# Performance work log

Measured on AMD Instinct MI355X. Metric: run time of the kernel, lower is better.

The kernel has to match this reference:

```python
import jax, jax.numpy as jnp
import numpy as np

N_NODES = 20000
N_EDGES = 320000
IN_DIM = 256
OUT_DIM = 256
N_HEADS = 4
D_K = OUT_DIM // N_HEADS
N_NTYPES = 4
N_RELS = 8
SQRT_DK = float(np.sqrt(D_K))


def setup_inputs() -> dict:
    key = jax.random.key(0)
    ks = jax.random.split(key, 12)
    xav = lambda k, shape, fan: jax.random.normal(k, shape, jnp.float32) * (1.0 / np.sqrt(fan))
    return {
        "h": jax.random.normal(ks[0], (N_NODES, IN_DIM), jnp.float32),
        "k_linears": xav(ks[1], (N_NTYPES, IN_DIM, OUT_DIM), IN_DIM),
        "q_linears": xav(ks[2], (N_NTYPES, IN_DIM, OUT_DIM), IN_DIM),
        "v_linears": xav(ks[3], (N_NTYPES, IN_DIM, OUT_DIM), IN_DIM),
        "a_linears": xav(ks[4], (N_NTYPES, OUT_DIM, OUT_DIM), OUT_DIM),
        "relation_att": xav(ks[5], (N_RELS, N_HEADS, D_K, D_K), D_K),
        "relation_msg": xav(ks[6], (N_RELS, N_HEADS, D_K, D_K), D_K),
        "relation_pri": jnp.ones((N_RELS, N_HEADS), jnp.float32),
        "skip": jnp.ones((N_NTYPES,), jnp.float32),
        "node_type": jax.random.randint(ks[7], (N_NODES,), 0, N_NTYPES),
        "etype": jnp.sort(jax.random.randint(ks[8], (N_EDGES,), 0, N_RELS)),
        "row_idx": jax.random.randint(ks[9], (N_EDGES,), 0, N_NODES),
        "col_idx": jax.random.randint(ks[10], (N_EDGES,), 0, N_NODES),
    }


def _typed_matmul(x, W, node_type):
    # x: [N, in], W: [T, in, out] -> per-node-type projection [N, out]
    all_t = jnp.einsum("ni,tio->tno", x, W)  # [T, N, out]
    return all_t[node_type, jnp.arange(x.shape[0])]


def reference(h, k_linears, q_linears, v_linears, a_linears,
              relation_att, relation_msg, relation_pri, skip,
              node_type, etype, row_idx, col_idx):
    n = h.shape[0]
    # per-node-type K/Q/V projections -> [N, H, d_k]
    k = _typed_matmul(h, k_linears, node_type).reshape(n, N_HEADS, D_K)
    q = _typed_matmul(h, q_linears, node_type).reshape(n, N_HEADS, D_K)
    v = _typed_matmul(h, v_linears, node_type).reshape(n, N_HEADS, D_K)

    # per-relation transforms computed at node granularity, gathered per edge
    q_att = jnp.einsum("nhd,rhde->rnhe", q, relation_att)  # [R, N, H, d_k]
    v_msg = jnp.einsum("nhd,rhde->rnhe", v, relation_msg)  # [R, N, H, d_k]

    aw_q_edge = q_att[etype, col_idx]   # [E, H, d_k]  (dst-side q transformed by rel att)
    msg_edge = v_msg[etype, row_idx]    # [E, H, d_k]  (src-side v transformed by rel msg)

    # attention score: <rel_att @ q_dst, k_src> * pri_r / sqrt(d_k)  -> [E, H]
    attn_score = jnp.sum(aw_q_edge * k[row_idx], axis=-1)
    score = attn_score * (relation_pri[etype] / SQRT_DK)

    # edge softmax over incoming edges of each destination node
    m = jax.ops.segment_max(score, col_idx, num_segments=n)       # [N, H]
    ex = jnp.exp(score - m[col_idx])                              # [E, H]
    denom = jax.ops.segment_sum(ex, col_idx, num_segments=n)      # [N, H]
    alpha = ex / denom[col_idx]                                   # [E, H]

    agg = jax.ops.segment_sum(alpha[..., None] * msg_edge, col_idx,
                              num_segments=n)                     # [N, H, d_k]
    agg = agg.reshape(n, OUT_DIM)

    # output per-node-type projection scaled by sigmoid(skip[type])
    out = _typed_matmul(agg, a_linears, node_type)
    out = jax.nn.sigmoid(skip)[node_type][:, None] * out
    return out
```

## Files before the change

### kernel.cpp

```cpp
#include <hip/hip_runtime.h>

static constexpr int NN  = 20000;
static constexpr int NE  = 320000;
static constexpr int NTY = 4;
static constexpr int NRL = 8;
static constexpr int NB  = NRL * NN;

static constexpr int ZB = (NB + NN * 4 + 255) / 256;
static constexpr int HB = NN * 64 / 256;
static constexpr int WB = 4 * 768;
static constexpr int AB = 4 * 256;
static constexpr int RB = 32 * 4096 / 256;
static constexpr int CB = (NN + 255) / 256;

typedef short bf16x8 __attribute__((ext_vector_type(8)));
typedef float f32x4  __attribute__((ext_vector_type(4)));
typedef unsigned short u16x4 __attribute__((ext_vector_type(4)));

__device__ __forceinline__ unsigned short f2bf(float f) {
  unsigned u = __float_as_uint(f);
  u += 0x7fffu + ((u >> 16) & 1u);
  return (unsigned short)(u >> 16);
}
__device__ __forceinline__ float bf2f(unsigned short b) {
  return __uint_as_float(((unsigned)b) << 16);
}
__device__ __forceinline__ f32x4 mfma16(bf16x8 a, bf16x8 b, f32x4 c) {
  return __builtin_amdgcn_mfma_f32_16x16x32_bf16(a, b, c, 0, 0, 0);
}

__global__ void k_tcount(const int* __restrict__ ntype, int* __restrict__ c4p) {
  __shared__ int c[4];
  if (threadIdx.x < 4) c[threadIdx.x] = 0;
  __syncthreads();
  int i = blockIdx.x * 256 + threadIdx.x;
  if (i < NN) atomicAdd(&c[ntype[i]], 1);
  __syncthreads();
  if (threadIdx.x < 4) c4p[blockIdx.x * 4 + threadIdx.x] = c[threadIdx.x];
}
__global__ void k_meta(const int* __restrict__ c4p, int* toff, int* ncur,
                       int* mt_t, int* mt_m, int* gcnt) {
  __shared__ int c4[4];
  __shared__ int ts[5];
  if (threadIdx.x < 4) {
    int s = 0;
    for (int b = 0; b < CB; ++b) s += c4p[b * 4 + threadIdx.x];
    c4[threadIdx.x] = s;
  }
  __syncthreads();
  if (threadIdx.x == 0) {
    int s = 0, s2 = 0;
    for (int t = 0; t < NTY; ++t) {
      toff[t] = s; ncur[t] = s; s += c4[t];
      ts[t] = s2; s2 += (c4[t] + 15) >> 4;
    }
    toff[NTY] = s; ts[NTY] = s2; gcnt[0] = s2;
  }
  __syncthreads();
  int nmt = ts[4];
  for (int i = threadIdx.x; i < nmt; i += 256) {
    int t = 0;
    while (t < 3 && i >= ts[t + 1]) ++t;
    mt_t[i] = t; mt_m[i] = i - ts[t];
  }
}
__global__ void k_nscatter(const int* __restrict__ key, int* cur,
                           int* nperm, int* inv) {
  int i = blockIdx.x * 256 + threadIdx.x;
  if (i < NN) {
    int p = atomicAdd(&cur[key[i]], 1);
    nperm[p] = i;
    inv[i] = p;
  }
}

__global__ void k_prep_all(const float* __restrict__ h, const float* __restrict__ Wk,
                           const float* __restrict__ Wq, const float* __restrict__ Wv,
                           const float* __restrict__ Wa, const float* __restrict__ ratt,
                           const float* __restrict__ rmsg, const int* __restrict__ nperm,
                           int* bcnt, float* denom,
                           unsigned short* hbp, unsigned short* Wt, unsigned short* At,
                           unsigned short* Att, unsigned short* Mt) {
  int b = blockIdx.x;
  if (b < ZB) {
    int i = b * 256 + threadIdx.x;
    if (i < NB) bcnt[i] = 0;
    else if (i < NB + NN * 4) denom[i - NB] = 0.f;
  } else if (b < ZB + HB) {
    int q = (b - ZB) * 256 + threadIdx.x;
    int p = q >> 6, c4 = q & 63;
    int node = nperm[p];
    const float* s = h + (size_t)node * 256 + c4 * 4;
    u16x4 o;
    o[0] = f2bf(s[0]); o[1] = f2bf(s[1]); o[2] = f2bf(s[2]); o[3] = f2bf(s[3]);
    *(u16x4*)(hbp + (size_t)p * 256 + c4 * 4) = o;
  } else if (b < ZB + HB + WB) {
    int bb = b - (ZB + HB);
    int j = bb % 768, t = bb / 768, i = threadIdx.x;
    const float* src; int c;
    if (j < 256)      { src = Wk; c = j; }
    else if (j < 512) { src = Wq; c = j - 256; }
    else              { src = Wv; c = j - 512; }
    Wt[(t * 768 + j) * 256 + i] = f2bf(src[(t * 256 + i) * 256 + c]);
  } else if (b < ZB + HB + WB + AB) {
    int bb = b - (ZB + HB + WB);
    int j = bb % 256, t = bb / 256, i = threadIdx.x;
    At[(t * 256 + j) * 256 + i] = f2bf(Wa[(t * 256 + i) * 256 + j]);
  } else {
    int idx = (b - (ZB + HB + WB + AB)) * 256 + threadIdx.x;
    int rh = idx >> 12, e = (idx >> 6) & 63, d = idx & 63;
    Att[idx] = f2bf(ratt[rh * 4096 + d * 64 + e]);
    Mt[idx]  = f2bf(rmsg[rh * 4096 + d * 64 + e]);
  }
}

__global__ void k_bcount(const int* __restrict__ etyp, const int* __restrict__ coli,
                         const int* __restrict__ inv, int* bcnt) {
  int e = blockIdx.x * 256 + threadIdx.x;
  if (e < NE) atomicAdd(&bcnt[etyp[e] * NN + inv[coli[e]]], 1);
}
__global__ void k_scan1(const int* cnt, int* off, int* psum) {
  __shared__ int sm[256];
  int i = blockIdx.x * 256 + threadIdx.x;
  int v = cnt[i];
  sm[threadIdx.x] = v;
  __syncthreads();
  for (int d = 1; d < 256; d <<= 1) {
    int t = (threadIdx.x >= d) ? sm[threadIdx.x - d] : 0;
    __syncthreads();
    sm[threadIdx.x] += t;
    __syncthreads();
  }
  off[i] = sm[threadIdx.x] - v;
  if (threadIdx.x == 255) psum[blockIdx.x] = sm[255];
}
__global__ void k_scan2(int* psum) {
  __shared__ int sm[1024];
  int t = threadIdx.x;
  int v = (t < 625) ? psum[t] : 0;
  sm[t] = v;
  __syncthreads();
  for (int d = 1; d < 1024; d <<= 1) {
    int x = (t >= d) ? sm[t - d] : 0;
    __syncthreads();
    sm[t] += x;
    __syncthreads();
  }
  if (t < 625) psum[t] = sm[t] - v;
}
__global__ void k_scan3(int* off, int* cur, const int* psum) {
  int i = blockIdx.x * 256 + threadIdx.x;
  int v = off[i] + psum[blockIdx.x];
  off[i] = v; cur[i] = v;
  if (i == 0) off[NB] = NE;
}
__global__ void k_escatter(const int* __restrict__ etyp, const int* __restrict__ rowi,
                           const int* __restrict__ coli, const int* __restrict__ inv,
                           int* cur, int* je) {
  int e = blockIdx.x * 256 + threadIdx.x;
  if (e >= NE) return;
  int bin = etyp[e] * NN + inv[coli[e]];
  int j = atomicAdd(&cur[bin], 1);
  je[j] = inv[rowi[e]];
}

__global__ __launch_bounds__(256) void k_gemm_kqv(
    const unsigned short* __restrict__ hbp, const unsigned short* __restrict__ Wt,
    const int* __restrict__ toff, const int* __restrict__ mt_t,
    const int* __restrict__ mt_m, const int* __restrict__ gcnt,
    unsigned short* __restrict__ kvb, unsigned short* __restrict__ qb) {
  int mtile = blockIdx.x;
  if (mtile >= gcnt[0]) return;
  int wave = threadIdx.x >> 6, lane = threadIdx.x & 63;
  int t = mt_t[mtile], tm = mt_m[mtile];
  int base = toff[t], cnt = toff[t + 1] - base;
  int lr = lane & 15, kq = lane >> 4;
  int arow = tm * 16 + lr;
  int prow = base + (arow < cnt ? arow : cnt - 1);
  const unsigned short* aptr = hbp + (size_t)prow * 256 + kq * 8;
  bf16x8 af[8];
#pragma unroll
  for (int s = 0; s < 8; ++s) af[s] = *(const bf16x8*)(aptr + s * 32);
  int pr[4]; bool wr[4];
#pragma unroll
  for (int i = 0; i < 4; ++i) {
    int crow = tm * 16 + kq * 4 + i;
    wr[i] = crow < cnt;
    pr[i] = base + (wr[i] ? crow : 0);
  }
  for (int j = 0; j < 12; ++j) {
    int tn = wave * 12 + j;
    const unsigned short* bptr = Wt + ((t * 768 + tn * 16 + lr) * 256) + kq * 8;
    f32x4 acc = {0.f, 0.f, 0.f, 0.f};
#pragma unroll
    for (int s = 0; s < 8; ++s)
      acc = mfma16(af[s], *(const bf16x8*)(bptr + s * 32), acc);
    int ccol = tn * 16 + lr;
#pragma unroll
    for (int i = 0; i < 4; ++i) {
      if (wr[i]) {
        unsigned short v = f2bf(acc[i]);
        if (ccol < 256)
          kvb[(size_t)pr[i] * 512 + (ccol >> 6) * 128 + (ccol & 63)] = v;
        else if (ccol < 512)
          qb[(size_t)pr[i] * 256 + (ccol - 256)] = v;
        else {
          int c = ccol - 512;
          kvb[(size_t)pr[i] * 512 + (c >> 6) * 128 + 64 + (c & 63)] = v;
        }
      }
    }
  }
}

__global__ __launch_bounds__(256) void k_mega(
    const int* __restrict__ boff, const int* __restrict__ je,
    const unsigned short* __restrict__ qb, const unsigned short* __restrict__ kvb,
    const unsigned short* __restrict__ Att, const unsigned short* __restrict__ Mt,
    const float* __restrict__ pri, unsigned short* __restrict__ aggh,
    float* __restrict__ denom) {
  __shared__ float qsh[4][32][68];
  int dt = blockIdx.x >> 2, quarter = blockIdx.x & 3;
  int h = threadIdx.x >> 6, lane = threadIdx.x & 63;
  int lr16 = lane & 15, kq4 = lane >> 4;
  int lr32 = lane & 31, kq1 = lane >> 5;
  int r0 = quarter * 2;
  float dtot = 0.f;
  f32x4 C[2][4] = {{{0.f,0.f,0.f,0.f},{0.f,0.f,0.f,0.f},{0.f,0.f,0.f,0.f},{0.f,0.f,0.f,0.f}},
                   {{0.f,0.f,0.f,0.f},{0.f,0.f,0.f,0.f},{0.f,0.f,0.f,0.f},{0.f,0.f,0.f,0.f}}};
  for (int rr = 0; rr < 2; ++rr) {
    int r = r0 + rr;
    int rh = r * 4 + h;
    int bin = r * NN + dt * 32 + lr32;
    int b0 = boff[bin], b1 = boff[bin + 1];
#pragma unroll
    for (int hf = 0; hf < 2; ++hf) {
      const unsigned short* ap = qb + (size_t)(dt * 32 + hf * 16 + lr16) * 256 + h * 64 + kq4 * 8;
      bf16x8 aq0 = *(const bf16x8*)ap;
      bf16x8 aq1 = *(const bf16x8*)(ap + 32);
#pragma unroll
      for (int tn = 0; tn < 4; ++tn) {
        const unsigned short* bp = Att + ((rh * 64 + tn * 16 + lr16) * 64) + kq4 * 8;
        f32x4 a = {0.f, 0.f, 0.f, 0.f};
        a = mfma16(aq0, *(const bf16x8*)bp, a);
        a = mfma16(aq1, *(const bf16x8*)(bp + 32), a);
#pragma unroll
        for (int i = 0; i < 4; ++i)
          qsh[h][hf * 16 + kq4 * 4 + i][tn * 16 + lr16] = a[i];
      }
    }
    float qt[32];
#pragma unroll
    for (int m = 0; m < 32; m += 4) {
      f32x4 v = *(const f32x4*)&qsh[h][lr32][kq1 * 32 + m];
      qt[m] = v[0]; qt[m + 1] = v[1]; qt[m + 2] = v[2]; qt[m + 3] = v[3];
    }
    float acc[32];
#pragma unroll
    for (int m = 0; m < 32; ++m) acc[m] = 0.f;
    float prs = pri[rh] * 0.125f;
    for (int j = b0; j < b1; ++j) {
      int src = je[j];
      const unsigned short* kp = kvb + (size_t)src * 512 + h * 128 + kq1 * 32;
      bf16x8 k0 = *(const bf16x8*)kp;
      bf16x8 k1 = *(const bf16x8*)(kp + 8);
      bf16x8 k2 = *(const bf16x8*)(kp + 16);
      bf16x8 k3 = *(const bf16x8*)(kp + 24);
      bf16x8 v0 = *(const bf16x8*)(kp + 64);
      bf16x8 v1 = *(const bf16x8*)(kp + 72);
      bf16x8 v2 = *(const bf16x8*)(kp + 80);
      bf16x8 v3 = *(const bf16x8*)(kp + 88);
      float s = 0.f;
#pragma unroll
      for (int m = 0; m < 8; ++m) {
        s += qt[m]      * bf2f((unsigned short)k0[m]);
        s += qt[8 + m]  * bf2f((unsigned short)k1[m]);
        s += qt[16 + m] * bf2f((unsigned short)k2[m]);
        s += qt[24 + m] * bf2f((unsigned short)k3[m]);
      }
      s += __shfl_xor(s, 32);
      float ex = __expf(s * prs);
      dtot += ex;
#pragma unroll
      for (int m = 0; m < 8; ++m) {
        acc[m]      += ex * bf2f((unsigned short)v0[m]);
        acc[8 + m]  += ex * bf2f((unsigned short)v1[m]);
        acc[16 + m] += ex * bf2f((unsigned short)v2[m]);
        acc[24 + m] += ex * bf2f((unsigned short)v3[m]);
      }
    }
#pragma unroll
    for (int m = 0; m < 32; m += 4) {
      f32x4 v = {acc[m], acc[m + 1], acc[m + 2], acc[m + 3]};
      *(f32x4*)&qsh[h][lr32][kq1 * 32 + m] = v;
    }
#pragma unroll
    for (int hf = 0; hf < 2; ++hf) {
      bf16x8 m0, m1;
#pragma unroll
      for (int m = 0; m < 8; ++m) {
        m0[m] = (short)f2bf(qsh[h][hf * 16 + lr16][kq4 * 8 + m]);
        m1[m] = (short)f2bf(qsh[h][hf * 16 + lr16][32 + kq4 * 8 + m]);
      }
#pragma unroll
      for (int tn = 0; tn < 4; ++tn) {
        const unsigned short* bp = Mt + ((rh * 64 + tn * 16 + lr16) * 64) + kq4 * 8;
        C[hf][tn] = mfma16(m0, *(const bf16x8*)bp, C[hf][tn]);
        C[hf][tn] = mfma16(m1, *(const bf16x8*)(bp + 32), C[hf][tn]);
      }
    }
  }
  if (kq1 == 0) atomicAdd(&denom[(dt * 32 + lr32) * 4 + h], dtot);
#pragma unroll
  for (int hf = 0; hf < 2; ++hf)
#pragma unroll
    for (int tn = 0; tn < 4; ++tn)
#pragma unroll
      for (int i = 0; i < 4; ++i)
        aggh[((size_t)quarter * NN + dt * 32 + hf * 16 + kq4 * 4 + i) * 256 +
             h * 64 + tn * 16 + lr16] = f2bf(C[hf][tn][i]);
}

__global__ __launch_bounds__(256) void k_gemm_out(
    const unsigned short* __restrict__ aggh, const float* __restrict__ denom,
    const unsigned short* __restrict__ At,
    const int* __restrict__ nperm, const int* __restrict__ toff,
    const int* __restrict__ mt_t, const int* __restrict__ mt_m,
    const int* __restrict__ gcnt,
    const float* __restrict__ skip, float* __restrict__ out) {
  int mtile = blockIdx.x;
  if (mtile >= gcnt[0]) return;
  int wave = threadIdx.x >> 6, lane = threadIdx.x & 63;
  int t = mt_t[mtile], tm = mt_m[mtile];
  int base = toff[t], cnt = toff[t + 1] - base;
  int lr = lane & 15, kq = lane >> 4;
  int arow = tm * 16 + lr;
  int prow = base + (arow < cnt ? arow : cnt - 1);
  float dn[4];
#pragma unroll
  for (int hh = 0; hh < 4; ++hh) {
    float d = denom[prow * 4 + hh];
    dn[hh] = d > 0.f ? 1.f / d : 0.f;
  }
  const unsigned short* g = aggh + (size_t)prow * 256 + kq * 8;
  bf16x8 af[8];
#pragma unroll
  for (int s = 0; s < 8; ++s) {
    bf16x8 x0 = *(const bf16x8*)(g + s * 32);
    bf16x8 x1 = *(const bf16x8*)(g + (size_t)NN * 256 + s * 32);
    bf16x8 x2 = *(const bf16x8*)(g + (size_t)2 * NN * 256 + s * 32);
    bf16x8 x3 = *(const bf16x8*)(g + (size_t)3 * NN * 256 + s * 32);
    float dv = dn[(kq * 8 + s * 32) >> 6];
#pragma unroll
    for (int m = 0; m < 8; ++m)
      af[s][m] = (short)f2bf((bf2f((unsigned short)x0[m]) + bf2f((unsigned short)x1[m]) +
                              bf2f((unsigned short)x2[m]) + bf2f((unsigned short)x3[m])) * dv);
  }
  int nd[4]; bool wr[4];
#pragma unroll
  for (int i = 0; i < 4; ++i) {
    int crow = tm * 16 + kq * 4 + i;
    wr[i] = crow < cnt;
    nd[i] = nperm[base + (wr[i] ? crow : 0)];
  }
  float sg = 1.f / (1.f + __expf(-skip[t]));
  for (int j = 0; j < 4; ++j) {
    int tn = wave * 4 + j;
    const unsigned short* bptr = At + (t * 256 + tn * 16 + lr) * 256 + kq * 8;
    f32x4 acc = {0.f, 0.f, 0.f, 0.f};
#pragma unroll
    for (int s = 0; s < 8; ++s)
      acc = mfma16(af[s], *(const bf16x8*)(bptr + s * 32), acc);
    int ccol = tn * 16 + lr;
#pragma unroll
    for (int i = 0; i < 4; ++i)
      if (wr[i]) out[nd[i] * 256 + ccol] = acc[i] * sg;
  }
}

extern "C" void kernel_launch(void* const* d_in, const int* in_sizes, int n_in,
                              void* d_out, int out_size, void* d_ws, size_t ws_size,
                              hipStream_t stream) {
  (void)in_sizes; (void)n_in; (void)out_size; (void)ws_size;
  const float* h    = (const float*)d_in[0];
  const float* Wk   = (const float*)d_in[1];
  const float* Wq   = (const float*)d_in[2];
  const float* Wv   = (const float*)d_in[3];
  const float* Wa   = (const float*)d_in[4];
  const float* ratt = (const float*)d_in[5];
  const float* rmsg = (const float*)d_in[6];
  const float* pri  = (const float*)d_in[7];
  const float* skp  = (const float*)d_in[8];
  const int* ntype  = (const int*)d_in[9];
  const int* etyp   = (const int*)d_in[10];
  const int* rowi   = (const int*)d_in[11];
  const int* coli   = (const int*)d_in[12];
  float* out = (float*)d_out;

  char* p = (char*)d_ws;
  auto alloc = [&](size_t bytes) {
    void* q = (void*)p;
    p += (bytes + 255) & ~(size_t)255;
    return q;
  };
  unsigned short* hbp  = (unsigned short*)alloc((size_t)NN * 256 * 2);
  unsigned short* Wt   = (unsigned short*)alloc((size_t)4 * 768 * 256 * 2);
  unsigned short* At   = (unsigned short*)alloc((size_t)4 * 256 * 256 * 2);
  unsigned short* Att  = (unsigned short*)alloc((size_t)32 * 4096 * 2);
  unsigned short* Mt   = (unsigned short*)alloc((size_t)32 * 4096 * 2);
  unsigned short* kvb  = (unsigned short*)alloc((size_t)NN * 512 * 2);
  unsigned short* qb   = (unsigned short*)alloc((size_t)NN * 256 * 2);
  unsigned short* aggh = (unsigned short*)alloc((size_t)4 * NN * 256 * 2);
  float* denom = (float*)alloc((size_t)NN * 4 * 4);
  int* toff  = (int*)alloc(32);
  int* ncur  = (int*)alloc(16);
  int* c4p   = (int*)alloc((size_t)CB * 4 * 4);
  int* nperm = (int*)alloc((size_t)NN * 4);
  int* inv   = (int*)alloc((size_t)NN * 4);
  int* bcnt  = (int*)alloc((size_t)NB * 4);
  int* boff  = (int*)alloc((size_t)(NB + 1) * 4);
  int* bcur  = (int*)alloc((size_t)NB * 4);
  int* psum  = (int*)alloc((size_t)625 * 4);
  int* je    = (int*)alloc((size_t)NE * 4);
  int* mt_t = (int*)alloc((size_t)1253 * 4);
  int* mt_m = (int*)alloc((size_t)1253 * 4);
  int* gcnt = (int*)alloc(32);

  k_tcount<<<CB, 256, 0, stream>>>(ntype, c4p);
  k_meta<<<1, 256, 0, stream>>>(c4p, toff, ncur, mt_t, mt_m, gcnt);
  k_nscatter<<<CB, 256, 0, stream>>>(ntype, ncur, nperm, inv);

  k_prep_all<<<ZB + HB + WB + AB + RB, 256, 0, stream>>>(
      h, Wk, Wq, Wv, Wa, ratt, rmsg, nperm, bcnt, denom, hbp, Wt, At, Att, Mt);

  k_bcount<<<(NE + 255) / 256, 256, 0, stream>>>(etyp, coli, inv, bcnt);
  k_scan1<<<625, 256, 0, stream>>>(bcnt, boff, psum);
  k_scan2<<<1, 1024, 0, stream>>>(psum);
  k_scan3<<<625, 256, 0, stream>>>(boff, bcur, psum);
  k_escatter<<<(NE + 255) / 256, 256, 0, stream>>>(etyp, rowi, coli, inv, bcur, je);

  k_gemm_kqv<<<1253, 256, 0, stream>>>(hbp, Wt, toff, mt_t, mt_m, gcnt, kvb, qb);
  k_mega<<<2500, 256, 0, stream>>>(boff, je, qb, kvb, Att, Mt, pri, aggh, denom);
  k_gemm_out<<<1253, 256, 0, stream>>>(aggh, denom, At, nperm, toff, mt_t, mt_m, gcnt,
                                       skp, out);
}
```

Before: 410.7 us.

## Use 64-row GEMM tiles with LDS-staged weights, fuse h conversion, bf16 LDS in mega

```diff
diff --git a/kernel.cpp b/kernel.cpp
--- a/kernel.cpp
+++ b/kernel.cpp
@@ -7,7 +7,6 @@
 static constexpr int NB  = NRL * NN;
 
 static constexpr int ZB = (NB + NN * 4 + 255) / 256;
-static constexpr int HB = NN * 64 / 256;
 static constexpr int WB = 4 * 768;
 static constexpr int AB = 4 * 256;
 static constexpr int RB = 32 * 4096 / 256;
@@ -39,7 +38,7 @@
   if (threadIdx.x < 4) c4p[blockIdx.x * 4 + threadIdx.x] = c[threadIdx.x];
 }
 __global__ void k_meta(const int* __restrict__ c4p, int* toff, int* ncur,
-                       int* mt_t, int* mt_m, int* gcnt) {
+                       int* mt64_t, int* mt64_m, int* gcnt) {
   __shared__ int c4[4];
   __shared__ int ts[5];
   if (threadIdx.x < 4) {
@@ -52,16 +51,16 @@
     int s = 0, s2 = 0;
     for (int t = 0; t < NTY; ++t) {
       toff[t] = s; ncur[t] = s; s += c4[t];
-      ts[t] = s2; s2 += (c4[t] + 15) >> 4;
+      ts[t] = s2; s2 += (c4[t] + 63) >> 6;
     }
     toff[NTY] = s; ts[NTY] = s2; gcnt[0] = s2;
   }
   __syncthreads();
-  int nmt = ts[4];
-  for (int i = threadIdx.x; i < nmt; i += 256) {
+  int n64 = ts[4];
+  for (int i = threadIdx.x; i < n64; i += 256) {
     int t = 0;
     while (t < 3 && i >= ts[t + 1]) ++t;
-    mt_t[i] = t; mt_m[i] = i - ts[t];
+    mt64_t[i] = t; mt64_m[i] = i - ts[t];
   }
 }
 __global__ void k_nscatter(const int* __restrict__ key, int* cur,
@@ -74,40 +73,32 @@
   }
 }
 
-__global__ void k_prep_all(const float* __restrict__ h, const float* __restrict__ Wk,
+__global__ void k_prep_all(const float* __restrict__ Wk,
                            const float* __restrict__ Wq, const float* __restrict__ Wv,
                            const float* __restrict__ Wa, const float* __restrict__ ratt,
-                           const float* __restrict__ rmsg, const int* __restrict__ nperm,
+                           const float* __restrict__ rmsg,
                            int* bcnt, float* denom,
-                           unsigned short* hbp, unsigned short* Wt, unsigned short* At,
+                           unsigned short* Wt, unsigned short* At,
                            unsigned short* Att, unsigned short* Mt) {
   int b = blockIdx.x;
   if (b < ZB) {
     int i = b * 256 + threadIdx.x;
     if (i < NB) bcnt[i] = 0;
     else if (i < NB + NN * 4) denom[i - NB] = 0.f;
-  } else if (b < ZB + HB) {
-    int q = (b - ZB) * 256 + threadIdx.x;
-    int p = q >> 6, c4 = q & 63;
-    int node = nperm[p];
-    const float* s = h + (size_t)node * 256 + c4 * 4;
-    u16x4 o;
-    o[0] = f2bf(s[0]); o[1] = f2bf(s[1]); o[2] = f2bf(s[2]); o[3] = f2bf(s[3]);
-    *(u16x4*)(hbp + (size_t)p * 256 + c4 * 4) = o;
-  } else if (b < ZB + HB + WB) {
-    int bb = b - (ZB + HB);
+  } else if (b < ZB + WB) {
+    int bb = b - ZB;
     int j = bb % 768, t = bb / 768, i = threadIdx.x;
     const float* src; int c;
     if (j < 256)      { src = Wk; c = j; }
     else if (j < 512) { src = Wq; c = j - 256; }
     else              { src = Wv; c = j - 512; }
     Wt[(t * 768 + j) * 256 + i] = f2bf(src[(t * 256 + i) * 256 + c]);
-  } else if (b < ZB + HB + WB + AB) {
-    int bb = b - (ZB + HB + WB);
+  } else if (b < ZB + WB + AB) {
+    int bb = b - (ZB + WB);
     int j = bb % 256, t = bb / 256, i = threadIdx.x;
     At[(t * 256 + j) * 256 + i] = f2bf(Wa[(t * 256 + i) * 256 + j]);
   } else {
-    int idx = (b - (ZB + HB + WB + AB)) * 256 + threadIdx.x;
+    int idx = (b - (ZB + WB + AB)) * 256 + threadIdx.x;
     int rh = idx >> 12, e = (idx >> 6) & 63, d = idx & 63;
     Att[idx] = f2bf(ratt[rh * 4096 + d * 64 + e]);
     Mt[idx]  = f2bf(rmsg[rh * 4096 + d * 64 + e]);
@@ -165,36 +156,53 @@
 }
 
 __global__ __launch_bounds__(256) void k_gemm_kqv(
-    const unsigned short* __restrict__ hbp, const unsigned short* __restrict__ Wt,
-    const int* __restrict__ toff, const int* __restrict__ mt_t,
-    const int* __restrict__ mt_m, const int* __restrict__ gcnt,
+    const float* __restrict__ hsrc, const unsigned short* __restrict__ Wt,
+    const int* __restrict__ nperm, const int* __restrict__ toff,
+    const int* __restrict__ mt64_t, const int* __restrict__ mt64_m,
+    const int* __restrict__ gcnt,
     unsigned short* __restrict__ kvb, unsigned short* __restrict__ qb) {
+  __shared__ unsigned short bs[16][264];
   int mtile = blockIdx.x;
   if (mtile >= gcnt[0]) return;
   int wave = threadIdx.x >> 6, lane = threadIdx.x & 63;
-  int t = mt_t[mtile], tm = mt_m[mtile];
+  int t = mt64_t[mtile], tm = mt64_m[mtile];
   int base = toff[t], cnt = toff[t + 1] - base;
   int lr = lane & 15, kq = lane >> 4;
-  int arow = tm * 16 + lr;
+  int arow = tm * 64 + wave * 16 + lr;
   int prow = base + (arow < cnt ? arow : cnt - 1);
-  const unsigned short* aptr = hbp + (size_t)prow * 256 + kq * 8;
+  int node = nperm[prow];
+  const float* ap = hsrc + (size_t)node * 256 + kq * 8;
   bf16x8 af[8];
 #pragma unroll
-  for (int s = 0; s < 8; ++s) af[s] = *(const bf16x8*)(aptr + s * 32);
+  for (int s = 0; s < 8; ++s) {
+    f32x4 x0 = *(const f32x4*)(ap + s * 32);
+    f32x4 x1 = *(const f32x4*)(ap + s * 32 + 4);
+    bf16x8 o;
+    o[0] = (short)f2bf(x0[0]); o[1] = (short)f2bf(x0[1]);
+    o[2] = (short)f2bf(x0[2]); o[3] = (short)f2bf(x0[3]);
+    o[4] = (short)f2bf(x1[0]); o[5] = (short)f2bf(x1[1]);
+    o[6] = (short)f2bf(x1[2]); o[7] = (short)f2bf(x1[3]);
+    af[s] = o;
+  }
   int pr[4]; bool wr[4];
 #pragma unroll
   for (int i = 0; i < 4; ++i) {
-    int crow = tm * 16 + kq * 4 + i;
+    int crow = tm * 64 + wave * 16 + kq * 4 + i;
     wr[i] = crow < cnt;
     pr[i] = base + (wr[i] ? crow : 0);
   }
-  for (int j = 0; j < 12; ++j) {
-    int tn = wave * 12 + j;
-    const unsigned short* bptr = Wt + ((t * 768 + tn * 16 + lr) * 256) + kq * 8;
+  int sc = threadIdx.x >> 4;
+  int seg = threadIdx.x & 15;
+  for (int tn = 0; tn < 48; ++tn) {
+    const unsigned short* wsrc = Wt + ((size_t)(t * 768 + tn * 16 + sc)) * 256 + seg * 16;
+    __syncthreads();
+    *(bf16x8*)&bs[sc][seg * 16]     = *(const bf16x8*)wsrc;
+    *(bf16x8*)&bs[sc][seg * 16 + 8] = *(const bf16x8*)(wsrc + 8);
+    __syncthreads();
     f32x4 acc = {0.f, 0.f, 0.f, 0.f};
 #pragma unroll
     for (int s = 0; s < 8; ++s)
-      acc = mfma16(af[s], *(const bf16x8*)(bptr + s * 32), acc);
+      acc = mfma16(af[s], *(const bf16x8*)&bs[lr][kq * 8 + s * 32], acc);
     int ccol = tn * 16 + lr;
 #pragma unroll
     for (int i = 0; i < 4; ++i) {
@@ -219,7 +227,7 @@
     const unsigned short* __restrict__ Att, const unsigned short* __restrict__ Mt,
     const float* __restrict__ pri, unsigned short* __restrict__ aggh,
     float* __restrict__ denom) {
-  __shared__ float qsh[4][32][68];
+  __shared__ unsigned short qsh[4][32][80];
   int dt = blockIdx.x >> 2, quarter = blockIdx.x & 3;
   int h = threadIdx.x >> 6, lane = threadIdx.x & 63;
   int lr16 = lane & 15, kq4 = lane >> 4;
@@ -246,15 +254,13 @@
         a = mfma16(aq1, *(const bf16x8*)(bp + 32), a);
 #pragma unroll
         for (int i = 0; i < 4; ++i)
-          qsh[h][hf * 16 + kq4 * 4 + i][tn * 16 + lr16] = a[i];
+          qsh[h][hf * 16 + kq4 * 4 + i][tn * 16 + lr16] = f2bf(a[i]);
       }
     }
-    float qt[32];
-#pragma unroll
-    for (int m = 0; m < 32; m += 4) {
-      f32x4 v = *(const f32x4*)&qsh[h][lr32][kq1 * 32 + m];
-      qt[m] = v[0]; qt[m + 1] = v[1]; qt[m + 2] = v[2]; qt[m + 3] = v[3];
-    }
+    bf16x8 qtp[4];
+#pragma unroll
+    for (int g = 0; g < 4; ++g)
+      qtp[g] = *(const bf16x8*)&qsh[h][lr32][kq1 * 32 + g * 8];
     float acc[32];
 #pragma unroll
     for (int m = 0; m < 32; ++m) acc[m] = 0.f;
@@ -273,10 +279,10 @@
       float s = 0.f;
 #pragma unroll
       for (int m = 0; m < 8; ++m) {
-        s += qt[m]      * bf2f((unsigned short)k0[m]);
-        s += qt[8 + m]  * bf2f((unsigned short)k1[m]);
-        s += qt[16 + m] * bf2f((unsigned short)k2[m]);
-        s += qt[24 + m] * bf2f((unsigned short)k3[m]);
+        s += bf2f((unsigned short)qtp[0][m]) * bf2f((unsigned short)k0[m]);
+        s += bf2f((unsigned short)qtp[1][m]) * bf2f((unsigned short)k1[m]);
+        s += bf2f((unsigned short)qtp[2][m]) * bf2f((unsigned short)k2[m]);
+        s += bf2f((unsigned short)qtp[3][m]) * bf2f((unsigned short)k3[m]);
       }
       s += __shfl_xor(s, 32);
       float ex = __expf(s * prs);
@@ -290,18 +296,16 @@
       }
     }
 #pragma unroll
-    for (int m = 0; m < 32; m += 4) {
-      f32x4 v = {acc[m], acc[m + 1], acc[m + 2], acc[m + 3]};
-      *(f32x4*)&qsh[h][lr32][kq1 * 32 + m] = v;
+    for (int g = 0; g < 4; ++g) {
+      bf16x8 o;
+#pragma unroll
+      for (int m = 0; m < 8; ++m) o[m] = (short)f2bf(acc[g * 8 + m]);
+      *(bf16x8*)&qsh[h][lr32][kq1 * 32 + g * 8] = o;
     }
 #pragma unroll
     for (int hf = 0; hf < 2; ++hf) {
-      bf16x8 m0, m1;
-#pragma unroll
-      for (int m = 0; m < 8; ++m) {
-        m0[m] = (short)f2bf(qsh[h][hf * 16 + lr16][kq4 * 8 + m]);
-        m1[m] = (short)f2bf(qsh[h][hf * 16 + lr16][32 + kq4 * 8 + m]);
-      }
+      bf16x8 m0 = *(const bf16x8*)&qsh[h][hf * 16 + lr16][kq4 * 8];
+      bf16x8 m1 = *(const bf16x8*)&qsh[h][hf * 16 + lr16][32 + kq4 * 8];
 #pragma unroll
       for (int tn = 0; tn < 4; ++tn) {
         const unsigned short* bp = Mt + ((rh * 64 + tn * 16 + lr16) * 64) + kq4 * 8;
@@ -325,16 +329,17 @@
     const unsigned short* __restrict__ aggh, const float* __restrict__ denom,
     const unsigned short* __restrict__ At,
     const int* __restrict__ nperm, const int* __restrict__ toff,
-    const int* __restrict__ mt_t, const int* __restrict__ mt_m,
+    const int* __restrict__ mt64_t, const int* __restrict__ mt64_m,
     const int* __restrict__ gcnt,
     const float* __restrict__ skip, float* __restrict__ out) {
+  __shared__ unsigned short bs[16][264];
   int mtile = blockIdx.x;
   if (mtile >= gcnt[0]) return;
   int wave = threadIdx.x >> 6, lane = threadIdx.x & 63;
-  int t = mt_t[mtile], tm = mt_m[mtile];
+  int t = mt64_t[mtile], tm = mt64_m[mtile];
   int base = toff[t], cnt = toff[t + 1] - base;
   int lr = lane & 15, kq = lane >> 4;
-  int arow = tm * 16 + lr;
+  int arow = tm * 64 + wave * 16 + lr;
   int prow = base + (arow < cnt ? arow : cnt - 1);
   float dn[4];
 #pragma unroll
@@ -359,18 +364,23 @@
   int nd[4]; bool wr[4];
 #pragma unroll
   for (int i = 0; i < 4; ++i) {
-    int crow = tm * 16 + kq * 4 + i;
+    int crow = tm * 64 + wave * 16 + kq * 4 + i;
     wr[i] = crow < cnt;
     nd[i] = nperm[base + (wr[i] ? crow : 0)];
   }
   float sg = 1.f / (1.f + __expf(-skip[t]));
-  for (int j = 0; j < 4; ++j) {
-    int tn = wave * 4 + j;
-    const unsigned short* bptr = At + (t * 256 + tn * 16 + lr) * 256 + kq * 8;
+  int sc = threadIdx.x >> 4;
+  int seg = threadIdx.x & 15;
+  for (int tn = 0; tn < 16; ++tn) {
+    const unsigned short* wsrc = At + ((size_t)(t * 256 + tn * 16 + sc)) * 256 + seg * 16;
+    __syncthreads();
+    *(bf16x8*)&bs[sc][seg * 16]     = *(const bf16x8*)wsrc;
+    *(bf16x8*)&bs[sc][seg * 16 + 8] = *(const bf16x8*)(wsrc + 8);
+    __syncthreads();
     f32x4 acc = {0.f, 0.f, 0.f, 0.f};
 #pragma unroll
     for (int s = 0; s < 8; ++s)
-      acc = mfma16(af[s], *(const bf16x8*)(bptr + s * 32), acc);
+      acc = mfma16(af[s], *(const bf16x8*)&bs[lr][kq * 8 + s * 32], acc);
     int ccol = tn * 16 + lr;
 #pragma unroll
     for (int i = 0; i < 4; ++i)
@@ -403,7 +413,6 @@
     p += (bytes + 255) & ~(size_t)255;
     return q;
   };
-  unsigned short* hbp  = (unsigned short*)alloc((size_t)NN * 256 * 2);
   unsigned short* Wt   = (unsigned short*)alloc((size_t)4 * 768 * 256 * 2);
   unsigned short* At   = (unsigned short*)alloc((size_t)4 * 256 * 256 * 2);
   unsigned short* Att  = (unsigned short*)alloc((size_t)32 * 4096 * 2);
@@ -412,26 +421,26 @@
   unsigned short* qb   = (unsigned short*)alloc((size_t)NN * 256 * 2);
   unsigned short* aggh = (unsigned short*)alloc((size_t)4 * NN * 256 * 2);
   float* denom = (float*)alloc((size_t)NN * 4 * 4);
-  int* toff  = (int*)alloc(32);
-  int* ncur  = (int*)alloc(16);
-  int* c4p   = (int*)alloc((size_t)CB * 4 * 4);
-  int* nperm = (int*)alloc((size_t)NN * 4);
-  int* inv   = (int*)alloc((size_t)NN * 4);
-  int* bcnt  = (int*)alloc((size_t)NB * 4);
-  int* boff  = (int*)alloc((size_t)(NB + 1) * 4);
-  int* bcur  = (int*)alloc((size_t)NB * 4);
-  int* psum  = (int*)alloc((size_t)625 * 4);
-  int* je    = (int*)alloc((size_t)NE * 4);
-  int* mt_t = (int*)alloc((size_t)1253 * 4);
-  int* mt_m = (int*)alloc((size_t)1253 * 4);
-  int* gcnt = (int*)alloc(32);
+  int* toff   = (int*)alloc(32);
+  int* ncur   = (int*)alloc(16);
+  int* c4p    = (int*)alloc((size_t)CB * 4 * 4);
+  int* nperm  = (int*)alloc((size_t)NN * 4);
+  int* inv    = (int*)alloc((size_t)NN * 4);
+  int* bcnt   = (int*)alloc((size_t)NB * 4);
+  int* boff   = (int*)alloc((size_t)(NB + 1) * 4);
+  int* bcur   = (int*)alloc((size_t)NB * 4);
+  int* psum   = (int*)alloc((size_t)625 * 4);
+  int* je     = (int*)alloc((size_t)NE * 4);
+  int* mt64_t = (int*)alloc((size_t)324 * 4);
+  int* mt64_m = (int*)alloc((size_t)324 * 4);
+  int* gcnt   = (int*)alloc(32);
 
   k_tcount<<<CB, 256, 0, stream>>>(ntype, c4p);
-  k_meta<<<1, 256, 0, stream>>>(c4p, toff, ncur, mt_t, mt_m, gcnt);
+  k_meta<<<1, 256, 0, stream>>>(c4p, toff, ncur, mt64_t, mt64_m, gcnt);
   k_nscatter<<<CB, 256, 0, stream>>>(ntype, ncur, nperm, inv);
 
-  k_prep_all<<<ZB + HB + WB + AB + RB, 256, 0, stream>>>(
-      h, Wk, Wq, Wv, Wa, ratt, rmsg, nperm, bcnt, denom, hbp, Wt, At, Att, Mt);
+  k_prep_all<<<ZB + WB + AB + RB, 256, 0, stream>>>(
+      Wk, Wq, Wv, Wa, ratt, rmsg, bcnt, denom, Wt, At, Att, Mt);
 
   k_bcount<<<(NE + 255) / 256, 256, 0, stream>>>(etyp, coli, inv, bcnt);
   k_scan1<<<625, 256, 0, stream>>>(bcnt, boff, psum);
@@ -439,8 +448,8 @@
   k_scan3<<<625, 256, 0, stream>>>(boff, bcur, psum);
   k_escatter<<<(NE + 255) / 256, 256, 0, stream>>>(etyp, rowi, coli, inv, bcur, je);
 
-  k_gemm_kqv<<<1253, 256, 0, stream>>>(hbp, Wt, toff, mt_t, mt_m, gcnt, kvb, qb);
+  k_gemm_kqv<<<320, 256, 0, stream>>>(h, Wt, nperm, toff, mt64_t, mt64_m, gcnt, kvb, qb);
   k_mega<<<2500, 256, 0, stream>>>(boff, je, qb, kvb, Att, Mt, pri, aggh, denom);
-  k_gemm_out<<<1253, 256, 0, stream>>>(aggh, denom, At, nperm, toff, mt_t, mt_m, gcnt,
-                                       skp, out);
-}
+  k_gemm_out<<<320, 256, 0, stream>>>(aggh, denom, At, nperm, toff, mt64_t, mt64_m, gcnt,
+                                      skp, out);
+}
```

New measurement: 376.4 us. -8.4%, faster.
